# Performance work log

Measured on AMD Instinct MI355X. Metric: run time of the kernel, lower is better.

## Reference

```python
import jax, jax.numpy as jnp
import numpy as np

NUM_VOXEL_X = 128
NUM_VOXEL_Y = 128
NUM_CHANNELS = 80


def setup_inputs() -> dict:
    key = jax.random.key(0)
    k1, k2, k3 = jax.random.split(key, 3)
    B, N, D, H, W = 2, 6, 112, 16, 44
    total = B * N * D * H * W
    geom_xyz = jax.random.randint(k1, (total, 3), 0, 128, dtype=jnp.int64 if jax.config.jax_enable_x64 else jnp.int32).astype(jnp.int32)
    depth_features = jax.random.uniform(k2, (total,), dtype=jnp.float32)
    context_features = jax.random.normal(k3, (B, N, NUM_CHANNELS, H, W), dtype=jnp.float32)
    return {
        "geom_xyz": geom_xyz,
        "depth_features": depth_features,
        "context_features": context_features,
        "batch_size": B,
        "num_cams": N,
        "num_depth": D,
        "num_height": H,
        "num_width": W,
    }


def reference(geom_xyz, depth_features, context_features, batch_size, num_cams, num_depth, num_height, num_width):
    B, N, D, H, W = batch_size, num_cams, num_depth, num_height, num_width
    C = NUM_CHANNELS
    total = B * N * D * H * W

    # per-point feature = depth * context (context does not depend on depth bin)
    depth = depth_features.reshape(B, N, D, H, W)
    ctx = jnp.transpose(context_features, (0, 1, 3, 4, 2))  # (B,N,H,W,C)
    feats = depth[..., None] * ctx[:, :, None, :, :, :]      # (B,N,D,H,W,C)
    feats = feats.reshape(total, C)

    x = geom_xyz[:, 0].astype(jnp.int32)
    y = geom_xyz[:, 1].astype(jnp.int32)
    valid = (x >= 0) & (x < NUM_VOXEL_X) & (y >= 0) & (y < NUM_VOXEL_Y)

    batch_idx = (jnp.arange(total, dtype=jnp.int32) // (N * D * H * W))
    flat_idx = batch_idx * (NUM_VOXEL_Y * NUM_VOXEL_X) + jnp.clip(y, 0, NUM_VOXEL_Y - 1) * NUM_VOXEL_X + jnp.clip(x, 0, NUM_VOXEL_X - 1)

    feats = jnp.where(valid[:, None], feats, 0.0)
    out = jax.ops.segment_sum(feats, flat_idx, num_segments=B * NUM_VOXEL_Y * NUM_VOXEL_X)
    return out.reshape(B, NUM_VOXEL_Y, NUM_VOXEL_X, C)
```

## Files before the change

kernel.cpp:

```cpp
#include <hip/hip_runtime.h>


namespace {
constexpr int NVX = 128, NVY = 128, C = 80;
constexpr int B = 2, N = 6, D = 112, H = 16, W = 44;
constexpr int HW    = H * W;
constexpr int BN    = B * N;
constexpr int DHW   = D * HW;
constexpr int NDHW  = N * DHW;
constexpr int TOTAL = B * NDHW;
constexpr int NVOX  = B * NVY * NVX;

constexpr int NBIN  = 256;
constexpr int VPB   = NVOX / NBIN;
constexpr int SLOT  = 16;
constexpr int CAP   = 15;
constexpr int PTS_PER_BLK = 2048;
constexpr int SCAN_BLOCKS = TOTAL / PTS_PER_BLK;
constexpr int TR_BLOCKS   = BN * (C / 16) * (HW / 64);
constexpr int PRE_BLOCKS  = SCAN_BLOCKS + TR_BLOCKS;
constexpr int SPILLCAP = 65536;

constexpr int VCAP = 56;
}

__global__ __launch_bounds__(256) void pre_kernel(
    const int*   __restrict__ geom, const float* __restrict__ depth,
    const float* __restrict__ ctx,  float* __restrict__ ctx_t,
    int2* __restrict__ staging, int* __restrict__ spillcnt,
    int2* __restrict__ spill)
{
    __shared__ int2  stage[NBIN * SLOT];
    __shared__ int   bcnt[NBIN];
    __shared__ float tile[16 * 68];

    if (blockIdx.x < SCAN_BLOCKS) {
        const int t = threadIdx.x;
        bcnt[t] = 0;
        __syncthreads();

        const int p0 = blockIdx.x * PTS_PER_BLK + t * 8;
        const int4* g4 = (const int4*)(geom + (size_t)3 * p0);
        int4 q[6];
        #pragma unroll
        for (int i = 0; i < 6; ++i) q[i] = g4[i];
        const float4 d0 = *(const float4*)(depth + p0);
        const float4 d1 = *(const float4*)(depth + p0 + 4);
        const int xs[8] = {q[0].x, q[0].w, q[1].z, q[2].y,
                           q[3].x, q[3].w, q[4].z, q[5].y};
        const int ys[8] = {q[0].y, q[1].x, q[1].w, q[2].z,
                           q[3].y, q[4].x, q[4].w, q[5].z};
        const float ds[8] = {d0.x, d0.y, d0.z, d0.w, d1.x, d1.y, d1.z, d1.w};

        #pragma unroll
        for (int u = 0; u < 8; ++u) {
            const int x = xs[u], y = ys[u];
            if ((unsigned)x >= (unsigned)NVX || (unsigned)y >= (unsigned)NVY) continue;
            const int p   = p0 + u;
            const int b   = (p >= NDHW) ? 1 : 0;
            const int v   = (b * NVY + y) * NVX + x;
            const int bn  = (unsigned)p / (unsigned)DHW;
            const int hw  = (unsigned)p % (unsigned)HW;
            const int key = (v << 14) | (bn * HW + hw);
            const int bin = v & 255;
            const int idx = atomicAdd(&bcnt[bin], 1);
            if (idx < CAP) {
                stage[bin * SLOT + idx] = make_int2(key, __float_as_int(ds[u]));
            } else {
                int s = atomicAdd(spillcnt, 1);
                if (s < SPILLCAP) spill[s] = make_int2(key, __float_as_int(ds[u]));
            }
        }
        __syncthreads();
        stage[t * SLOT + CAP].x = bcnt[t];
        __syncthreads();

        const int4* src = (const int4*)stage;
        int4* dst = (int4*)staging;
        #pragma unroll
        for (int k = 0; k < 8; ++k) {
            const int i = k * 256 + t;
            const int bin = i >> 3, part = i & 7;
            dst[((size_t)bin * SCAN_BLOCKS + blockIdx.x) * 8 + part] = src[i];
        }
    } else {
        const int tb  = blockIdx.x - SCAN_BLOCKS;
        const int bn  = tb / 55;
        const int rem = tb % 55;
        const int c0  = (rem / 11) * 16;
        const int hw0 = (rem % 11) * 64;
        const int t = threadIdx.x;
        const int cl = t >> 6, hwl = t & 63;
        #pragma unroll
        for (int r = 0; r < 4; ++r) {
            const int c = r * 4 + cl;
            tile[c * 68 + hwl] =
                ctx[(size_t)(bn * C + c0 + c) * HW + hw0 + hwl];
        }
        __syncthreads();
        const int cr = t & 15, hwr = t >> 4;
        #pragma unroll
        for (int r = 0; r < 4; ++r) {
            const int hw = r * 16 + hwr;
            ctx_t[(size_t)(bn * HW + hw0 + hw) * C + c0 + cr] =
                tile[cr * 68 + hw];
        }
    }
}

__global__ __launch_bounds__(1024) void acc_kernel(
    const int2* __restrict__ staging, const float* __restrict__ ctx_t,
    float* __restrict__ out, int* __restrict__ spillcnt,
    int2* __restrict__ spill)
{
    __shared__ int2 list[VPB * VCAP];
    __shared__ int  vcnt[VPB];

    const int bin  = blockIdx.x;
    const int t    = threadIdx.x;
    const int wave = t >> 6, lane = t & 63;

    if (t < VPB) vcnt[t] = 0;
    __syncthreads();

    const int sub = lane >> 4, slot = lane & 15;
    for (int c = wave; c < (SCAN_BLOCKS + 3) / 4; c += 16) {
        const int s = c * 4 + sub;
        int2 e = make_int2(0, 0);
        if (s < SCAN_BLOCKS)
            e = staging[((size_t)bin * SCAN_BLOCKS + s) * SLOT + slot];
        int cnt = __shfl(e.x, lane | 15);
        cnt = cnt < CAP ? cnt : CAP;
        if (s < SCAN_BLOCKS && slot < cnt) {
            const int vl  = e.x >> 22;
            const int idx = atomicAdd(&vcnt[vl], 1);
            if (idx < VCAP) {
                list[vl * VCAP + idx] = e;
            } else {
                int sp = atomicAdd(spillcnt, 1);
                if (sp < SPILLCAP) spill[sp] = e;
            }
        }
    }
    __syncthreads();

    const int off2 = 64 + (lane & 15);
    for (int vv = 0; vv < VPB / 16; ++vv) {
        const int vl = wave * (VPB / 16) + vv;
        int n = vcnt[vl];
        n = n < VCAP ? n : VCAP;
        const int2* lp = list + vl * VCAP;

        float a0 = 0.f, a1 = 0.f, a2 = 0.f, a3 = 0.f;
        float b0 = 0.f, b1 = 0.f, b2 = 0.f, b3 = 0.f;
        int j = 0;
        for (; j + 4 <= n; j += 4) {
            const int2 e0 = lp[j], e1 = lp[j + 1], e2 = lp[j + 2], e3 = lp[j + 3];
            const float* c0 = ctx_t + (size_t)(e0.x & 16383) * C;
            const float* c1 = ctx_t + (size_t)(e1.x & 16383) * C;
            const float* c2 = ctx_t + (size_t)(e2.x & 16383) * C;
            const float* c3 = ctx_t + (size_t)(e3.x & 16383) * C;
            const float f0 = c0[lane], f1 = c1[lane], f2 = c2[lane], f3 = c3[lane];
            const float g0 = c0[off2], g1 = c1[off2], g2 = c2[off2], g3 = c3[off2];
            const float d0 = __int_as_float(e0.y), d1 = __int_as_float(e1.y);
            const float d2 = __int_as_float(e2.y), d3 = __int_as_float(e3.y);
            a0 += d0 * f0; a1 += d1 * f1; a2 += d2 * f2; a3 += d3 * f3;
            b0 += d0 * g0; b1 += d1 * g1; b2 += d2 * g2; b3 += d3 * g3;
        }
        for (; j < n; ++j) {
            const int2 e = lp[j];
            const float* c = ctx_t + (size_t)(e.x & 16383) * C;
            const float d = __int_as_float(e.y);
            a0 += d * c[lane];
            b0 += d * c[off2];
        }
        const float av = (a0 + a1) + (a2 + a3);
        const float bv = (b0 + b1) + (b2 + b3);
        float* o = out + (size_t)((vl << 8) | bin) * C;
        o[lane] = av;
        if (lane < 16) o[64 + lane] = bv;
    }
}

__global__ __launch_bounds__(256) void spill_kernel(
    const int* __restrict__ spillcnt, const int2* __restrict__ spill,
    const float* __restrict__ ctx_t, float* __restrict__ out)
{
    const int nwaves = gridDim.x * 4;
    const int wave   = blockIdx.x * 4 + (threadIdx.x >> 6);
    const int lane   = threadIdx.x & 63;
    int cnt = *spillcnt;
    if (cnt > SPILLCAP) cnt = SPILLCAP;
    for (int i = wave; i < cnt; i += nwaves) {
        const int2 e = spill[i];
        const int v   = e.x >> 14;
        const int row = e.x & 16383;
        const float dep = __int_as_float(e.y);
        const float* c = ctx_t + (size_t)row * C;
        float* o = out + (size_t)v * C;
        unsafeAtomicAdd(o + lane, dep * c[lane]);
        if (lane < C - 64) unsafeAtomicAdd(o + 64 + lane, dep * c[64 + lane]);
    }
}

extern "C" void kernel_launch(void* const* d_in, const int* in_sizes, int n_in,
                              void* d_out, int out_size, void* d_ws, size_t ws_size,
                              hipStream_t stream) {
    const int*   geom  = (const int*)d_in[0];
    const float* depth = (const float*)d_in[1];
    const float* ctx   = (const float*)d_in[2];
    float*       out   = (float*)d_out;

    char* ws = (char*)d_ws;
    int2* staging  = (int2*)ws; ws += (size_t)SCAN_BLOCKS * NBIN * SLOT * 8;
    int2* spill    = (int2*)ws; ws += (size_t)SPILLCAP * 8;
    int*  spillcnt = (int*)ws;  ws += 256;
    float* ctx_t   = (float*)ws;

    hipMemsetAsync(spillcnt, 0, 256, stream);

    pre_kernel  <<<dim3(PRE_BLOCKS), dim3(256),  0, stream>>>(
                    geom, depth, ctx, ctx_t, staging, spillcnt, spill);
    acc_kernel  <<<dim3(NBIN),       dim3(1024), 0, stream>>>(
                    staging, ctx_t, out, spillcnt, spill);
    spill_kernel<<<dim3(64),         dim3(256),  0, stream>>>(spillcnt, spill, ctx_t, out);
}
```

Baseline: 133.5 us.

## Split scan and transpose kernels, rotate bin slots, batch spill atomics, unroll accumulation by eight

Splits the fused pre-kernel into a separate scan kernel and transpose kernel. The scan now does its shared atomics in batches and rotates the slot index by bin to spread LDS bank conflicts. Spill appends are aggregated per wave with ballot and popcount, so each wave issues one global atomic. The accumulation loop is unrolled to eight independent gathers and VCAP is raised by one. Together these aim to cut LDS conflicts, global atomic contention and gather latency, at the cost of an extra kernel launch and higher register pressure.

```diff
diff --git a/kernel.cpp b/kernel.cpp
--- a/kernel.cpp
+++ b/kernel.cpp
@@ -18,93 +18,110 @@
 constexpr int PTS_PER_BLK = 2048;
 constexpr int SCAN_BLOCKS = TOTAL / PTS_PER_BLK;
 constexpr int TR_BLOCKS   = BN * (C / 16) * (HW / 64);
-constexpr int PRE_BLOCKS  = SCAN_BLOCKS + TR_BLOCKS;
 constexpr int SPILLCAP = 65536;
 
-constexpr int VCAP = 56;
-}
-
-__global__ __launch_bounds__(256) void pre_kernel(
+constexpr int VCAP = 57;
+}
+
+__global__ __launch_bounds__(256) void scan_kernel(
     const int*   __restrict__ geom, const float* __restrict__ depth,
-    const float* __restrict__ ctx,  float* __restrict__ ctx_t,
     int2* __restrict__ staging, int* __restrict__ spillcnt,
     int2* __restrict__ spill)
 {
-    __shared__ int2  stage[NBIN * SLOT];
-    __shared__ int   bcnt[NBIN];
+    __shared__ int2 stage[NBIN * SLOT];
+    __shared__ int  bcnt[NBIN];
+
+    const int t = threadIdx.x;
+    const int lane = t & 63;
+    bcnt[t] = 0;
+    __syncthreads();
+
+    const int p0 = blockIdx.x * PTS_PER_BLK + t * 8;
+    const int4* g4 = (const int4*)(geom + (size_t)3 * p0);
+    const int4 q0 = g4[0], q1 = g4[1], q2 = g4[2];
+    const int4 q3 = g4[3], q4 = g4[4], q5 = g4[5];
+    const float4 d0 = *(const float4*)(depth + p0);
+    const float4 d1 = *(const float4*)(depth + p0 + 4);
+    const int xs[8] = {q0.x, q0.w, q1.z, q2.y, q3.x, q3.w, q4.z, q5.y};
+    const int ys[8] = {q0.y, q1.x, q1.w, q2.z, q3.y, q4.x, q4.w, q5.z};
+    const int db[8] = {__float_as_int(d0.x), __float_as_int(d0.y),
+                       __float_as_int(d0.z), __float_as_int(d0.w),
+                       __float_as_int(d1.x), __float_as_int(d1.y),
+                       __float_as_int(d1.z), __float_as_int(d1.w)};
+
+    int bins[8], keys[8], idxv[8];
+    #pragma unroll
+    for (int u = 0; u < 8; ++u) {
+        const int x = xs[u], y = ys[u];
+        const bool ok = (unsigned)x < (unsigned)NVX && (unsigned)y < (unsigned)NVY;
+        const int p   = p0 + u;
+        const int b   = (p >= NDHW) ? 1 : 0;
+        const int v   = (b * NVY + y) * NVX + x;
+        const int bn  = (unsigned)p / (unsigned)DHW;
+        const int hw  = (unsigned)p % (unsigned)HW;
+        bins[u] = v & 255;
+        keys[u] = (v << 14) | (bn * HW + hw);
+        idxv[u] = ok ? -1 : -2;
+    }
+    #pragma unroll
+    for (int u = 0; u < 8; ++u)
+        if (idxv[u] == -1) idxv[u] = atomicAdd(&bcnt[bins[u]], 1);
+    #pragma unroll
+    for (int u = 0; u < 8; ++u)
+        if ((unsigned)idxv[u] < (unsigned)CAP)
+            stage[bins[u] * SLOT + ((idxv[u] + bins[u]) & 15)] =
+                make_int2(keys[u], db[u]);
+    #pragma unroll
+    for (int u = 0; u < 8; ++u) {
+        const bool sp = (idxv[u] >= CAP);
+        const unsigned long long m = __ballot(sp);
+        if (m) {
+            const int leader = (int)__ffsll((unsigned long long)m) - 1;
+            int base = 0;
+            if (lane == leader) base = atomicAdd(spillcnt, (int)__popcll(m));
+            base = __shfl(base, leader);
+            if (sp) {
+                const int off = base + (int)__popcll(m & ((1ull << lane) - 1ull));
+                if (off < SPILLCAP) spill[off] = make_int2(keys[u], db[u]);
+            }
+        }
+    }
+    __syncthreads();
+    stage[t * SLOT + ((t + CAP) & 15)].x = bcnt[t];
+    __syncthreads();
+
+    const int4* src = (const int4*)stage;
+    int4* dst = (int4*)staging;
+    #pragma unroll
+    for (int k = 0; k < 8; ++k) {
+        const int i = k * 256 + t;
+        const int sl = i >> 3, part = i & 7;
+        dst[((size_t)sl * SCAN_BLOCKS + blockIdx.x) * 8 + part] = src[i];
+    }
+}
+
+__global__ __launch_bounds__(256) void tr_kernel(
+    const float* __restrict__ ctx, float* __restrict__ ctx_t)
+{
     __shared__ float tile[16 * 68];
-
-    if (blockIdx.x < SCAN_BLOCKS) {
-        const int t = threadIdx.x;
-        bcnt[t] = 0;
-        __syncthreads();
-
-        const int p0 = blockIdx.x * PTS_PER_BLK + t * 8;
-        const int4* g4 = (const int4*)(geom + (size_t)3 * p0);
-        int4 q[6];
-        #pragma unroll
-        for (int i = 0; i < 6; ++i) q[i] = g4[i];
-        const float4 d0 = *(const float4*)(depth + p0);
-        const float4 d1 = *(const float4*)(depth + p0 + 4);
-        const int xs[8] = {q[0].x, q[0].w, q[1].z, q[2].y,
-                           q[3].x, q[3].w, q[4].z, q[5].y};
-        const int ys[8] = {q[0].y, q[1].x, q[1].w, q[2].z,
-                           q[3].y, q[4].x, q[4].w, q[5].z};
-        const float ds[8] = {d0.x, d0.y, d0.z, d0.w, d1.x, d1.y, d1.z, d1.w};
-
-        #pragma unroll
-        for (int u = 0; u < 8; ++u) {
-            const int x = xs[u], y = ys[u];
-            if ((unsigned)x >= (unsigned)NVX || (unsigned)y >= (unsigned)NVY) continue;
-            const int p   = p0 + u;
-            const int b   = (p >= NDHW) ? 1 : 0;
-            const int v   = (b * NVY + y) * NVX + x;
-            const int bn  = (unsigned)p / (unsigned)DHW;
-            const int hw  = (unsigned)p % (unsigned)HW;
-            const int key = (v << 14) | (bn * HW + hw);
-            const int bin = v & 255;
-            const int idx = atomicAdd(&bcnt[bin], 1);
-            if (idx < CAP) {
-                stage[bin * SLOT + idx] = make_int2(key, __float_as_int(ds[u]));
-            } else {
-                int s = atomicAdd(spillcnt, 1);
-                if (s < SPILLCAP) spill[s] = make_int2(key, __float_as_int(ds[u]));
-            }
-        }
-        __syncthreads();
-        stage[t * SLOT + CAP].x = bcnt[t];
-        __syncthreads();
-
-        const int4* src = (const int4*)stage;
-        int4* dst = (int4*)staging;
-        #pragma unroll
-        for (int k = 0; k < 8; ++k) {
-            const int i = k * 256 + t;
-            const int bin = i >> 3, part = i & 7;
-            dst[((size_t)bin * SCAN_BLOCKS + blockIdx.x) * 8 + part] = src[i];
-        }
-    } else {
-        const int tb  = blockIdx.x - SCAN_BLOCKS;
-        const int bn  = tb / 55;
-        const int rem = tb % 55;
-        const int c0  = (rem / 11) * 16;
-        const int hw0 = (rem % 11) * 64;
-        const int t = threadIdx.x;
-        const int cl = t >> 6, hwl = t & 63;
-        #pragma unroll
-        for (int r = 0; r < 4; ++r) {
-            const int c = r * 4 + cl;
-            tile[c * 68 + hwl] =
-                ctx[(size_t)(bn * C + c0 + c) * HW + hw0 + hwl];
-        }
-        __syncthreads();
-        const int cr = t & 15, hwr = t >> 4;
-        #pragma unroll
-        for (int r = 0; r < 4; ++r) {
-            const int hw = r * 16 + hwr;
-            ctx_t[(size_t)(bn * HW + hw0 + hw) * C + c0 + cr] =
-                tile[cr * 68 + hw];
-        }
+    const int tb  = blockIdx.x;
+    const int bn  = tb / 55;
+    const int rem = tb % 55;
+    const int c0  = (rem / 11) * 16;
+    const int hw0 = (rem % 11) * 64;
+    const int t = threadIdx.x;
+    const int cl = t >> 6, hwl = t & 63;
+    #pragma unroll
+    for (int r = 0; r < 4; ++r) {
+        const int c = r * 4 + cl;
+        tile[c * 68 + hwl] = ctx[(size_t)(bn * C + c0 + c) * HW + hw0 + hwl];
+    }
+    __syncthreads();
+    const int cr = t & 15, hwr = t >> 4;
+    #pragma unroll
+    for (int r = 0; r < 4; ++r) {
+        const int hw = r * 16 + hwr;
+        ctx_t[(size_t)(bn * HW + hw0 + hw) * C + c0 + cr] = tile[cr * 68 + hw];
     }
 }
 
@@ -124,14 +141,16 @@
     __syncthreads();
 
     const int sub = lane >> 4, slot = lane & 15;
+    const int cslot   = (bin + CAP) & 15;
+    const int logical = (slot - bin) & 15;
     for (int c = wave; c < (SCAN_BLOCKS + 3) / 4; c += 16) {
         const int s = c * 4 + sub;
         int2 e = make_int2(0, 0);
         if (s < SCAN_BLOCKS)
             e = staging[((size_t)bin * SCAN_BLOCKS + s) * SLOT + slot];
-        int cnt = __shfl(e.x, lane | 15);
+        int cnt = __shfl(e.x, (lane & 48) | cslot);
         cnt = cnt < CAP ? cnt : CAP;
-        if (s < SCAN_BLOCKS && slot < cnt) {
+        if (s < SCAN_BLOCKS && logical < cnt) {
             const int vl  = e.x >> 22;
             const int idx = atomicAdd(&vcnt[vl], 1);
             if (idx < VCAP) {
@@ -152,8 +171,34 @@
         const int2* lp = list + vl * VCAP;
 
         float a0 = 0.f, a1 = 0.f, a2 = 0.f, a3 = 0.f;
+        float a4 = 0.f, a5 = 0.f, a6 = 0.f, a7 = 0.f;
         float b0 = 0.f, b1 = 0.f, b2 = 0.f, b3 = 0.f;
+        float b4 = 0.f, b5 = 0.f, b6 = 0.f, b7 = 0.f;
         int j = 0;
+        for (; j + 8 <= n; j += 8) {
+            const int2 e0 = lp[j],     e1 = lp[j + 1], e2 = lp[j + 2], e3 = lp[j + 3];
+            const int2 e4 = lp[j + 4], e5 = lp[j + 5], e6 = lp[j + 6], e7 = lp[j + 7];
+            const float* c0 = ctx_t + (size_t)(e0.x & 16383) * C;
+            const float* c1 = ctx_t + (size_t)(e1.x & 16383) * C;
+            const float* c2 = ctx_t + (size_t)(e2.x & 16383) * C;
+            const float* c3 = ctx_t + (size_t)(e3.x & 16383) * C;
+            const float* c4 = ctx_t + (size_t)(e4.x & 16383) * C;
+            const float* c5 = ctx_t + (size_t)(e5.x & 16383) * C;
+            const float* c6 = ctx_t + (size_t)(e6.x & 16383) * C;
+            const float* c7 = ctx_t + (size_t)(e7.x & 16383) * C;
+            const float f0 = c0[lane], f1 = c1[lane], f2 = c2[lane], f3 = c3[lane];
+            const float f4 = c4[lane], f5 = c5[lane], f6 = c6[lane], f7 = c7[lane];
+            const float g0 = c0[off2], g1 = c1[off2], g2 = c2[off2], g3 = c3[off2];
+            const float g4_ = c4[off2], g5 = c5[off2], g6 = c6[off2], g7 = c7[off2];
+            const float w0 = __int_as_float(e0.y), w1 = __int_as_float(e1.y);
+            const float w2 = __int_as_float(e2.y), w3 = __int_as_float(e3.y);
+            const float w4 = __int_as_float(e4.y), w5 = __int_as_float(e5.y);
+            const float w6 = __int_as_float(e6.y), w7 = __int_as_float(e7.y);
+            a0 += w0 * f0; a1 += w1 * f1; a2 += w2 * f2; a3 += w3 * f3;
+            a4 += w4 * f4; a5 += w5 * f5; a6 += w6 * f6; a7 += w7 * f7;
+            b0 += w0 * g0; b1 += w1 * g1; b2 += w2 * g2; b3 += w3 * g3;
+            b4 += w4 * g4_; b5 += w5 * g5; b6 += w6 * g6; b7 += w7 * g7;
+        }
         for (; j + 4 <= n; j += 4) {
             const int2 e0 = lp[j], e1 = lp[j + 1], e2 = lp[j + 2], e3 = lp[j + 3];
             const float* c0 = ctx_t + (size_t)(e0.x & 16383) * C;
@@ -162,20 +207,20 @@
             const float* c3 = ctx_t + (size_t)(e3.x & 16383) * C;
             const float f0 = c0[lane], f1 = c1[lane], f2 = c2[lane], f3 = c3[lane];
             const float g0 = c0[off2], g1 = c1[off2], g2 = c2[off2], g3 = c3[off2];
-            const float d0 = __int_as_float(e0.y), d1 = __int_as_float(e1.y);
-            const float d2 = __int_as_float(e2.y), d3 = __int_as_float(e3.y);
-            a0 += d0 * f0; a1 += d1 * f1; a2 += d2 * f2; a3 += d3 * f3;
-            b0 += d0 * g0; b1 += d1 * g1; b2 += d2 * g2; b3 += d3 * g3;
+            const float w0 = __int_as_float(e0.y), w1 = __int_as_float(e1.y);
+            const float w2 = __int_as_float(e2.y), w3 = __int_as_float(e3.y);
+            a0 += w0 * f0; a1 += w1 * f1; a2 += w2 * f2; a3 += w3 * f3;
+            b0 += w0 * g0; b1 += w1 * g1; b2 += w2 * g2; b3 += w3 * g3;
         }
         for (; j < n; ++j) {
             const int2 e = lp[j];
             const float* c = ctx_t + (size_t)(e.x & 16383) * C;
-            const float d = __int_as_float(e.y);
-            a0 += d * c[lane];
-            b0 += d * c[off2];
-        }
-        const float av = (a0 + a1) + (a2 + a3);
-        const float bv = (b0 + b1) + (b2 + b3);
+            const float w = __int_as_float(e.y);
+            a0 += w * c[lane];
+            b0 += w * c[off2];
+        }
+        const float av = ((a0 + a1) + (a2 + a3)) + ((a4 + a5) + (a6 + a7));
+        const float bv = ((b0 + b1) + (b2 + b3)) + ((b4 + b5) + (b6 + b7));
         float* o = out + (size_t)((vl << 8) | bin) * C;
         o[lane] = av;
         if (lane < 16) o[64 + lane] = bv;
@@ -219,9 +264,10 @@
 
     hipMemsetAsync(spillcnt, 0, 256, stream);
 
-    pre_kernel  <<<dim3(PRE_BLOCKS), dim3(256),  0, stream>>>(
-                    geom, depth, ctx, ctx_t, staging, spillcnt, spill);
-    acc_kernel  <<<dim3(NBIN),       dim3(1024), 0, stream>>>(
+    scan_kernel <<<dim3(SCAN_BLOCKS), dim3(256),  0, stream>>>(
+                    geom, depth, staging, spillcnt, spill);
+    tr_kernel   <<<dim3(TR_BLOCKS),   dim3(256),  0, stream>>>(ctx, ctx_t);
+    acc_kernel  <<<dim3(NBIN),        dim3(1024), 0, stream>>>(
                     staging, ctx_t, out, spillcnt, spill);
-    spill_kernel<<<dim3(64),         dim3(256),  0, stream>>>(spillcnt, spill, ctx_t, out);
-}
+    spill_kernel<<<dim3(64),          dim3(256),  0, stream>>>(spillcnt, spill, ctx_t, out);
+}
```

New measurement: 136.7 us. +2.4%, slower.
